# Optimization experiments

Measured on AMD Instinct MI355X. Metric: run time of the kernel, lower is better.

## Reference

```python
import jax, jax.numpy as jnp
import numpy as np

NUM_LEVELS = 4
RADIUS = 4


def _avg_pool2(x):
    # 2x2 stride-2 average pool over the last two dims of a 5D array, VALID padding
    s = jax.lax.reduce_window(x, 0.0, jax.lax.add, (1, 1, 1, 2, 2), (1, 1, 1, 2, 2), 'VALID')
    return s / 4.0


def _forward(fmap1, fmap2, coords):
    B, C, Hf, Wf = fmap1.shape
    _, N, _, H, W = coords.shape
    K = 2 * RADIUS + 1

    # all-pairs correlation: (B, H1, W1, H2, W2), scaled by 1/sqrt(C)
    f1 = fmap1.reshape(B, C, Hf * Wf)
    f2 = fmap2.reshape(B, C, Hf * Wf)
    corr = jnp.einsum('bcp,bcq->bpq', f1, f2) / jnp.sqrt(jnp.asarray(C, fmap1.dtype))
    corr = corr.reshape(B, Hf, Wf, Hf, Wf)

    pyramid = [corr]
    c = corr
    for _ in range(NUM_LEVELS - 1):
        c = _avg_pool2(c)
        pyramid.append(c)

    # coords channels: 0 = x, 1 = y  ->  (B, N, H, W, 2)
    cf = jnp.moveaxis(coords, 2, -1)

    d = jnp.linspace(-RADIUS, RADIUS, K, dtype=corr.dtype)
    # matches torch.stack(torch.meshgrid(dy, dx, indexing='ij'), axis=-1)
    delta = jnp.stack(jnp.meshgrid(d, d, indexing='ij'), axis=-1)  # (K, K, 2)

    bi = jnp.arange(B)[:, None, None, None, None]
    hi = jnp.arange(H)[None, None, :, None, None]
    wi = jnp.arange(W)[None, None, None, :, None]

    outs = []
    for i, cl in enumerate(pyramid):
        h2, w2 = cl.shape[-2], cl.shape[-1]
        # sampling coords (B, N, H, W, K, K, 2)
        sc = cf[..., None, None, :] / (2.0 ** i) + delta
        # grid_sample(align_corners=True) with coords pre-clamped to [-1,1]
        # == bilinear sample with pixel coords clamped to the valid range
        x = jnp.clip(sc[..., 0], 0.0, w2 - 1)
        y = jnp.clip(sc[..., 1], 0.0, h2 - 1)
        x0 = jnp.floor(x)
        y0 = jnp.floor(y)
        fx = (x - x0).reshape(B, N, H, W, K * K)
        fy = (y - y0).reshape(B, N, H, W, K * K)
        x0i = x0.astype(jnp.int32).reshape(B, N, H, W, K * K)
        y0i = y0.astype(jnp.int32).reshape(B, N, H, W, K * K)
        x1i = jnp.minimum(x0i + 1, w2 - 1)  # weight fx is 0 at the boundary
        y1i = jnp.minimum(y0i + 1, h2 - 1)

        cl_flat = cl.reshape(B, H, W, h2 * w2)  # query grid == feature grid (H==Hf, W==Wf)

        def gather(yi, xi):
            idx = yi * w2 + xi  # (B, N, H, W, K*K)
            return cl_flat[bi, hi, wi, idx]

        v = (gather(y0i, x0i) * (1 - fy) * (1 - fx)
             + gather(y0i, x1i) * (1 - fy) * fx
             + gather(y1i, x0i) * fy * (1 - fx)
             + gather(y1i, x1i) * fy * fx)
        outs.append(v)  # (B, N, H, W, K*K)

    out = jnp.concatenate(outs, axis=-1)  # (B, N, H, W, num_levels*K*K)
    # torch: (B,N,H,W,Cc).reshape(B, N*Cc, H, W) -- a raw row-major reshape
    out = out.reshape(B, N * out.shape[-1], H, W)
    return out.astype(jnp.float32)


def setup_inputs() -> dict:
    key = jax.random.key(0)
    k1, k2, k3 = jax.random.split(key, 3)
    B, C, H, W, N = 2, 256, 64, 64, 8
    fmap1 = jax.random.normal(k1, (B, C, H, W), dtype=jnp.float32)
    fmap2 = jax.random.normal(k2, (B, C, H, W), dtype=jnp.float32)
    coords = jax.random.uniform(k3, (B, N, 2, H, W), dtype=jnp.float32) * (W - 1)
    return {"fmap1": fmap1, "fmap2": fmap2, "coords": coords}


def reference(fmap1, fmap2, coords):
    return _forward(fmap1, fmap2, coords)
```

## Files before the change

kernel.cpp:

```cpp
#include <hip/hip_runtime.h>
#include <hip/hip_bf16.h>
#include <stdint.h>

#define B_   2
#define C_   256
#define P_   4096
#define N_   8
#define OUTC 2592

typedef __bf16 bf16x8 __attribute__((ext_vector_type(8)));
typedef float floatx4 __attribute__((ext_vector_type(4)));

__device__ __forceinline__ float bf2f(unsigned int u16) {
    union { unsigned int i; float f; } x; x.i = u16 << 16; return x.f;
}
__device__ __forceinline__ unsigned int f2bf(float f) {
    union { float f; unsigned int i; } x; x.f = f;
    unsigned int u = x.i + 0x7FFFu + ((x.i >> 16) & 1u);
    return u >> 16;
}

__global__ void conv_both(const float* __restrict__ in1, const float* __restrict__ in2,
                          __hip_bfloat16* __restrict__ out1, __hip_bfloat16* __restrict__ out2) {
    __shared__ float tile[32][33];
    int which = blockIdx.z >> 1;
    int b  = blockIdx.z & 1;
    const float* in = which ? in2 : in1;
    __hip_bfloat16* out = which ? out2 : out1;
    int p0 = blockIdx.x * 32;
    int c0 = blockIdx.y * 32;
    int tx = threadIdx.x;
    int ty0 = threadIdx.y;
    const float* ip = in + ((size_t)b * C_ + c0) * P_ + p0;
    for (int r = 0; r < 4; r++) {
        int ty = ty0 + r * 8;
        tile[ty][tx] = ip[(size_t)ty * P_ + tx];
    }
    __syncthreads();
    __hip_bfloat16* op = out + ((size_t)b * P_ + p0) * C_ + c0;
    for (int r = 0; r < 4; r++) {
        int ty = ty0 + r * 8;
        op[(size_t)ty * C_ + tx] = __float2bfloat16(tile[tx][ty]);
    }
}

__global__ __launch_bounds__(256) void gemm_corr(const __hip_bfloat16* __restrict__ A,
                                                 const __hip_bfloat16* __restrict__ Bm,
                                                 unsigned short* __restrict__ Cmat) {
    __shared__ __align__(16) __hip_bfloat16 lA[128 * 32];
    __shared__ __align__(16) __hip_bfloat16 lB[128 * 32];
    const int id = blockIdx.x;
    const int bz = id >> 10;
    const int r_ = id & 1023;
    const int s_ = r_ >> 3;
    const int by = (r_ & 7) * 4 + (s_ >> 5);
    const int bx = s_ & 31;
    const int m0 = by * 128;
    const int n0 = bx * 128;
    const __hip_bfloat16* Ab = A  + (size_t)bz * P_ * C_;
    const __hip_bfloat16* Bb = Bm + (size_t)bz * P_ * C_;
    unsigned short* Cb = Cmat + (size_t)bz * P_ * P_;

    const int tid  = threadIdx.x;
    const int lane = tid & 63;
    const int w    = tid >> 6;
    const int wm   = w & 1, wn = w >> 1;

    floatx4 acc[4][4];
    for (int i = 0; i < 4; i++)
        for (int j = 0; j < 4; j++)
            acc[i][j] = floatx4{0.f, 0.f, 0.f, 0.f};

    const int srow = w * 16 + (lane >> 2);
    const int scol = (lane & 3) * 8;

    for (int k0 = 0; k0 < C_; k0 += 32) {
        for (int j = 0; j < 2; j++) {
            int row = j * 64 + srow;
            const __hip_bfloat16* ga = Ab + (size_t)(m0 + row) * C_ + k0 + scol;
            const __hip_bfloat16* gb = Bb + (size_t)(n0 + row) * C_ + k0 + scol;
            __hip_bfloat16* la = lA + (j * 64 + w * 16) * 32;
            __hip_bfloat16* lb = lB + (j * 64 + w * 16) * 32;
            __builtin_amdgcn_global_load_lds((const __attribute__((address_space(1))) void*)ga,
                                             (__attribute__((address_space(3))) void*)la, 16, 0, 0);
            __builtin_amdgcn_global_load_lds((const __attribute__((address_space(1))) void*)gb,
                                             (__attribute__((address_space(3))) void*)lb, 16, 0, 0);
        }
        __syncthreads();
        const int kq   = (lane >> 4) * 8;
        const int rsel = lane & 15;
        bf16x8 af[4], bfv[4];
        for (int i = 0; i < 4; i++) {
            af[i]  = *(const bf16x8*)&lA[(wm * 64 + i * 16 + rsel) * 32 + kq];
            bfv[i] = *(const bf16x8*)&lB[(wn * 64 + i * 16 + rsel) * 32 + kq];
        }
        for (int i = 0; i < 4; i++)
            for (int j = 0; j < 4; j++)
                acc[i][j] = __builtin_amdgcn_mfma_f32_16x16x32_bf16(af[i], bfv[j], acc[i][j], 0, 0, 0);
        __syncthreads();
    }

    const float scale = 0.0625f;
    const int colb  = n0 + wn * 64 + (lane & 15);
    const int rbase = m0 + wm * 64 + ((lane >> 4) * 4);
    for (int i = 0; i < 4; i++)
        for (int j = 0; j < 4; j++)
            for (int r = 0; r < 4; r++)
                Cb[(size_t)(rbase + i * 16 + r) * P_ + colb + j * 16] =
                    (unsigned short)f2bf(acc[i][j][r] * scale);
}

__global__ __launch_bounds__(256) void pyramid(const unsigned int* __restrict__ c0,
                                               unsigned int* __restrict__ c1,
                                               unsigned int* __restrict__ c2,
                                               unsigned int* __restrict__ c3) {
    __shared__ unsigned int L0[2048];
    __shared__ unsigned int L1[512];
    __shared__ unsigned int L2[128];
    const int bp = blockIdx.x;
    const int tid = threadIdx.x;
    {
        const uint2* g = (const uint2*)(c0 + (size_t)bp * 2048);
        uint2* d = (uint2*)L0;
        for (int i = tid; i < 1024; i += 256) d[i] = g[i];
    }
    __syncthreads();
    for (int t = tid; t < 512; t += 256) {
        int x = t & 15;
        int y = t >> 4;
        unsigned int a = L0[(2 * y) * 32 + 2 * x];
        unsigned int a2 = L0[(2 * y) * 32 + 2 * x + 1];
        unsigned int b = L0[(2 * y + 1) * 32 + 2 * x];
        unsigned int b2 = L0[(2 * y + 1) * 32 + 2 * x + 1];
        float s0 = 0.25f * (bf2f(a & 0xffff) + bf2f(a >> 16) + bf2f(b & 0xffff) + bf2f(b >> 16));
        float s1 = 0.25f * (bf2f(a2 & 0xffff) + bf2f(a2 >> 16) + bf2f(b2 & 0xffff) + bf2f(b2 >> 16));
        unsigned int u = f2bf(s0) | (f2bf(s1) << 16);
        L1[t] = u;
        c1[(size_t)bp * 512 + t] = u;
    }
    __syncthreads();
    if (tid < 128) {
        int x = tid & 7;
        int y = tid >> 3;
        unsigned int a = L1[(2 * y) * 16 + 2 * x];
        unsigned int a2 = L1[(2 * y) * 16 + 2 * x + 1];
        unsigned int b = L1[(2 * y + 1) * 16 + 2 * x];
        unsigned int b2 = L1[(2 * y + 1) * 16 + 2 * x + 1];
        float s0 = 0.25f * (bf2f(a & 0xffff) + bf2f(a >> 16) + bf2f(b & 0xffff) + bf2f(b >> 16));
        float s1 = 0.25f * (bf2f(a2 & 0xffff) + bf2f(a2 >> 16) + bf2f(b2 & 0xffff) + bf2f(b2 >> 16));
        unsigned int u = f2bf(s0) | (f2bf(s1) << 16);
        L2[tid] = u;
        c2[(size_t)bp * 128 + tid] = u;
    }
    __syncthreads();
    if (tid < 32) {
        int x = tid & 3;
        int y = tid >> 2;
        unsigned int a = L2[(2 * y) * 8 + 2 * x];
        unsigned int a2 = L2[(2 * y) * 8 + 2 * x + 1];
        unsigned int b = L2[(2 * y + 1) * 8 + 2 * x];
        unsigned int b2 = L2[(2 * y + 1) * 8 + 2 * x + 1];
        float s0 = 0.25f * (bf2f(a & 0xffff) + bf2f(a >> 16) + bf2f(b & 0xffff) + bf2f(b >> 16));
        float s1 = 0.25f * (bf2f(a2 & 0xffff) + bf2f(a2 >> 16) + bf2f(b2 & 0xffff) + bf2f(b2 >> 16));
        c3[(size_t)bp * 32 + tid] = f2bf(s0) | (f2bf(s1) << 16);
    }
}

__global__ __launch_bounds__(256) void sample_k(const unsigned short* __restrict__ c0,
                                                const unsigned short* __restrict__ c1,
                                                const unsigned short* __restrict__ c2,
                                                const unsigned short* __restrict__ c3,
                                                const float* __restrict__ coords,
                                                float* __restrict__ outp) {
    __shared__ unsigned short sl16[5680];
    __shared__ float cs[16];
    __shared__ float2 xt[288];
    __shared__ float2 yt[288];
    __shared__ unsigned int ctb[324];

    const int bp = blockIdx.x;
    const int b  = bp >> 12;
    const int p  = bp & 4095;
    const int tid = threadIdx.x;
    unsigned int* slu = (unsigned int*)sl16;

    {
        const uint2* g0 = (const uint2*)(c0 + (size_t)bp * 4096);
        for (int i = tid; i < 1024; i += 256) {
            uint2 v = g0[i];
            int e = 4 * i;
            int y = e >> 6, x = e & 63;
            int u = (y * 66 + x) >> 1;
            slu[u] = v.x; slu[u + 1] = v.y;
        }
        const unsigned int* g1 = (const unsigned int*)(c1 + (size_t)bp * 1024);
        for (int i = tid; i < 512; i += 256)
            slu[2112 + (i >> 4) * 17 + (i & 15)] = g1[i];
        if (tid < 128)
            slu[2656 + (tid >> 3) * 9 + (tid & 7)] =
                ((const unsigned int*)(c2 + (size_t)bp * 256))[tid];
        if (tid < 32)
            slu[2800 + (tid >> 2) * 5 + (tid & 3)] =
                ((const unsigned int*)(c3 + (size_t)bp * 64))[tid];
        if (tid < 16) cs[tid] = coords[(size_t)(b * 16 + tid) * 4096 + p];
    }
    __syncthreads();

    for (int t = tid; t < 324; t += 256) {
        if (t < 288) {
            int n = t / 36, rem = t - n * 36;
            int l = rem / 9, dd = rem - l * 9;
            int wl = 64 >> l;
            int pw   = (l == 0) ? 66 : (l == 1) ? 34 : (l == 2) ? 18 : 10;
            int base = (l == 0) ? 0  : (l == 1) ? 4224 : (l == 2) ? 5312 : 5600;
            float inv = 1.0f / (float)(1 << l);
            float mx = (float)(wl - 1);
            float cx = cs[n * 2 + 0], cy = cs[n * 2 + 1];
            float xx = fminf(fmaxf(cx * inv + (float)(dd - 4), 0.0f), mx);
            float yy = fminf(fmaxf(cy * inv + (float)(dd - 4), 0.0f), mx);
            float x0f = floorf(xx), y0f = floorf(yy);
            int x0 = (int)x0f, y0 = (int)y0f;
            int x1 = min(x0 + 1, wl - 1), y1 = min(y0 + 1, wl - 1);
            unsigned int xb = (unsigned int)x0 | ((unsigned int)x1 << 8);
            unsigned int yb = (unsigned int)(base + y0 * pw)
                            | ((unsigned int)(base + y1 * pw) << 16);
            xt[t] = make_float2(xx - x0f, __uint_as_float(xb));
            yt[t] = make_float2(yy - y0f, __uint_as_float(yb));
        }
        int c = t;
        int l = c / 81, k = c - l * 81;
        int i9 = k / 9, j9 = k - i9 * 9;
        ctb[c] = ((unsigned int)(l * 9 + i9) << 8) | (unsigned int)(l * 9 + j9);
    }
    __syncthreads();

    const size_t outbase = (size_t)b * ((size_t)N_ * P_ * 324) + (size_t)p * 324;
    for (int o = tid; o < OUTC; o += 256) {
        int n = o / 324;
        int c = o - n * 324;
        unsigned int cv = ctb[c];
        int tb = n * 36;
        float2 xv = xt[tb + (cv >> 8)];
        float2 yv = yt[tb + (cv & 255)];
        unsigned int xb = __float_as_uint(xv.y);
        unsigned int yb = __float_as_uint(yv.y);
        int x0 = xb & 255, x1 = xb >> 8;
        int r0 = yb & 0xffff, r1 = yb >> 16;
        float fx = xv.x, fy = yv.x;
        float v00 = bf2f(sl16[r0 + x0]);
        float v01 = bf2f(sl16[r0 + x1]);
        float v10 = bf2f(sl16[r1 + x0]);
        float v11 = bf2f(sl16[r1 + x1]);
        float vx0 = v00 + fx * (v01 - v00);
        float vx1 = v10 + fx * (v11 - v10);
        float v   = vx0 + fy * (vx1 - vx0);
        outp[outbase + (size_t)n * (324 * 4095) + o] = v;
    }
}

extern "C" void kernel_launch(void* const* d_in, const int* in_sizes, int n_in,
                              void* d_out, int out_size, void* d_ws, size_t ws_size,
                              hipStream_t stream) {
    const float* fmap1  = (const float*)d_in[0];
    const float* fmap2  = (const float*)d_in[1];
    const float* coords = (const float*)d_in[2];
    float* out = (float*)d_out;

    char* ws = (char*)d_ws;
    size_t off = 0;
    auto alloc = [&](size_t bytes) {
        void* ptr = ws + off;
        off += (bytes + 255) & ~(size_t)255;
        return ptr;
    };
    __hip_bfloat16* f1t = (__hip_bfloat16*)alloc((size_t)B_ * P_ * C_ * 2);
    __hip_bfloat16* f2t = (__hip_bfloat16*)alloc((size_t)B_ * P_ * C_ * 2);
    unsigned short* corr0 = (unsigned short*)alloc((size_t)B_ * P_ * 4096 * 2);
    unsigned short* corr1 = (unsigned short*)alloc((size_t)B_ * P_ * 1024 * 2);
    unsigned short* corr2 = (unsigned short*)alloc((size_t)B_ * P_ * 256 * 2);
    unsigned short* corr3 = (unsigned short*)alloc((size_t)B_ * P_ * 64 * 2);

    conv_both<<<dim3(128, 8, 2 * B_), dim3(32, 8), 0, stream>>>(fmap1, fmap2, f1t, f2t);

    gemm_corr<<<dim3(2048), dim3(256), 0, stream>>>(f1t, f2t, corr0);

    pyramid<<<dim3(B_ * P_), dim3(256), 0, stream>>>((const unsigned int*)corr0,
                                                     (unsigned int*)corr1,
                                                     (unsigned int*)corr2,
                                                     (unsigned int*)corr3);

    sample_k<<<dim3(B_ * P_), dim3(256), 0, stream>>>(corr0, corr1, corr2, corr3, coords, out);
}
```

Baseline: 180.2 us.

## Fuse first pyramid pooling level into GEMM epilogue with packed bf16 stores

The correlation GEMM's warp tiling changes so each wave covers 32 rows by 128 columns, making horizontally adjacent column pairs reachable with a lane shuffle. The epilogue writes level-0 as packed 32-bit bf16 pairs and computes the level-1 2x2 average directly, so the pyramid kernel no longer rereads the full level-0 correlation volume. The remaining pyramid kernel only builds levels 2 and 3 from level 1. The sampling loop also replaces a per-iteration divide by 324 with an incremental counter. The level-1 value is now averaged from fp32 accumulators rather than rounded bf16, which slightly changes rounding.

```diff
diff --git a/kernel.cpp b/kernel.cpp
--- a/kernel.cpp
+++ b/kernel.cpp
@@ -46,7 +46,8 @@
 
 __global__ __launch_bounds__(256) void gemm_corr(const __hip_bfloat16* __restrict__ A,
                                                  const __hip_bfloat16* __restrict__ Bm,
-                                                 unsigned short* __restrict__ Cmat) {
+                                                 unsigned int* __restrict__ C0,
+                                                 unsigned short* __restrict__ C1) {
     __shared__ __align__(16) __hip_bfloat16 lA[128 * 32];
     __shared__ __align__(16) __hip_bfloat16 lB[128 * 32];
     const int id = blockIdx.x;
@@ -59,16 +60,14 @@
     const int n0 = bx * 128;
     const __hip_bfloat16* Ab = A  + (size_t)bz * P_ * C_;
     const __hip_bfloat16* Bb = Bm + (size_t)bz * P_ * C_;
-    unsigned short* Cb = Cmat + (size_t)bz * P_ * P_;
 
     const int tid  = threadIdx.x;
     const int lane = tid & 63;
     const int w    = tid >> 6;
-    const int wm   = w & 1, wn = w >> 1;
-
-    floatx4 acc[4][4];
-    for (int i = 0; i < 4; i++)
-        for (int j = 0; j < 4; j++)
+
+    floatx4 acc[2][8];
+    for (int i = 0; i < 2; i++)
+        for (int j = 0; j < 8; j++)
             acc[i][j] = floatx4{0.f, 0.f, 0.f, 0.f};
 
     const int srow = w * 16 + (lane >> 2);
@@ -89,62 +88,64 @@
         __syncthreads();
         const int kq   = (lane >> 4) * 8;
         const int rsel = lane & 15;
-        bf16x8 af[4], bfv[4];
-        for (int i = 0; i < 4; i++) {
-            af[i]  = *(const bf16x8*)&lA[(wm * 64 + i * 16 + rsel) * 32 + kq];
-            bfv[i] = *(const bf16x8*)&lB[(wn * 64 + i * 16 + rsel) * 32 + kq];
-        }
-        for (int i = 0; i < 4; i++)
-            for (int j = 0; j < 4; j++)
-                acc[i][j] = __builtin_amdgcn_mfma_f32_16x16x32_bf16(af[i], bfv[j], acc[i][j], 0, 0, 0);
+        bf16x8 af[2];
+        for (int i = 0; i < 2; i++)
+            af[i] = *(const bf16x8*)&lA[(w * 32 + i * 16 + rsel) * 32 + kq];
+        for (int jh = 0; jh < 2; jh++) {
+            bf16x8 bfv[4];
+            for (int jj = 0; jj < 4; jj++)
+                bfv[jj] = *(const bf16x8*)&lB[((jh * 4 + jj) * 16 + rsel) * 32 + kq];
+            for (int i = 0; i < 2; i++)
+                for (int jj = 0; jj < 4; jj++)
+                    acc[i][jh * 4 + jj] =
+                        __builtin_amdgcn_mfma_f32_16x16x32_bf16(af[i], bfv[jj],
+                                                                acc[i][jh * 4 + jj], 0, 0, 0);
+        }
         __syncthreads();
     }
 
     const float scale = 0.0625f;
-    const int colb  = n0 + wn * 64 + (lane & 15);
-    const int rbase = m0 + wm * 64 + ((lane >> 4) * 4);
-    for (int i = 0; i < 4; i++)
-        for (int j = 0; j < 4; j++)
-            for (int r = 0; r < 4; r++)
-                Cb[(size_t)(rbase + i * 16 + r) * P_ + colb + j * 16] =
-                    (unsigned short)f2bf(acc[i][j][r] * scale);
-}
-
-__global__ __launch_bounds__(256) void pyramid(const unsigned int* __restrict__ c0,
-                                               unsigned int* __restrict__ c1,
-                                               unsigned int* __restrict__ c2,
-                                               unsigned int* __restrict__ c3) {
-    __shared__ unsigned int L0[2048];
+    const int s15  = lane & 15;
+    const int even = (lane & 1) == 0;
+    for (int i = 0; i < 2; i++) {
+        for (int r = 0; r < 4; r++) {
+            int rp = m0 + w * 32 + i * 16 + ((lane >> 4) & 3) * 4 + r;
+            size_t rb0 = ((size_t)bz * P_ + rp) * 2048;
+            size_t rb1 = ((size_t)bz * P_ + rp) * 1024 + bx * 32;
+            for (int j = 0; j < 4; j++) {
+                float v0 = acc[i][j][r] * scale;
+                float v1 = acc[i][j + 4][r] * scale;
+                float v0n = __shfl_xor(v0, 1);
+                float v1n = __shfl_xor(v1, 1);
+                unsigned int u = even ? (f2bf(v0) | (f2bf(v0n) << 16))
+                                      : (f2bf(v1n) | (f2bf(v1) << 16));
+                int colu = even ? ((n0 + j * 16 + s15) >> 1)
+                                : ((n0 + j * 16 + 64 + s15 - 1) >> 1);
+                C0[rb0 + colu] = u;
+                if (even) {
+                    float s4 = (v0 + v0n + v1 + v1n) * 0.25f;
+                    C1[rb1 + ((j * 16 + s15) >> 1)] = (unsigned short)f2bf(s4);
+                }
+            }
+        }
+    }
+}
+
+__global__ __launch_bounds__(256) void pyr23(const unsigned int* __restrict__ c1,
+                                             unsigned int* __restrict__ c2,
+                                             unsigned int* __restrict__ c3) {
     __shared__ unsigned int L1[512];
     __shared__ unsigned int L2[128];
     const int bp = blockIdx.x;
     const int tid = threadIdx.x;
-    {
-        const uint2* g = (const uint2*)(c0 + (size_t)bp * 2048);
-        uint2* d = (uint2*)L0;
-        for (int i = tid; i < 1024; i += 256) d[i] = g[i];
-    }
-    __syncthreads();
-    for (int t = tid; t < 512; t += 256) {
-        int x = t & 15;
-        int y = t >> 4;
-        unsigned int a = L0[(2 * y) * 32 + 2 * x];
-        unsigned int a2 = L0[(2 * y) * 32 + 2 * x + 1];
-        unsigned int b = L0[(2 * y + 1) * 32 + 2 * x];
-        unsigned int b2 = L0[(2 * y + 1) * 32 + 2 * x + 1];
-        float s0 = 0.25f * (bf2f(a & 0xffff) + bf2f(a >> 16) + bf2f(b & 0xffff) + bf2f(b >> 16));
-        float s1 = 0.25f * (bf2f(a2 & 0xffff) + bf2f(a2 >> 16) + bf2f(b2 & 0xffff) + bf2f(b2 >> 16));
-        unsigned int u = f2bf(s0) | (f2bf(s1) << 16);
-        L1[t] = u;
-        c1[(size_t)bp * 512 + t] = u;
-    }
+    L1[tid]       = c1[(size_t)bp * 512 + tid];
+    L1[tid + 256] = c1[(size_t)bp * 512 + tid + 256];
     __syncthreads();
     if (tid < 128) {
-        int x = tid & 7;
-        int y = tid >> 3;
-        unsigned int a = L1[(2 * y) * 16 + 2 * x];
+        int x = tid & 7, y = tid >> 3;
+        unsigned int a  = L1[(2 * y) * 16 + 2 * x];
         unsigned int a2 = L1[(2 * y) * 16 + 2 * x + 1];
-        unsigned int b = L1[(2 * y + 1) * 16 + 2 * x];
+        unsigned int b  = L1[(2 * y + 1) * 16 + 2 * x];
         unsigned int b2 = L1[(2 * y + 1) * 16 + 2 * x + 1];
         float s0 = 0.25f * (bf2f(a & 0xffff) + bf2f(a >> 16) + bf2f(b & 0xffff) + bf2f(b >> 16));
         float s1 = 0.25f * (bf2f(a2 & 0xffff) + bf2f(a2 >> 16) + bf2f(b2 & 0xffff) + bf2f(b2 >> 16));
@@ -154,11 +155,10 @@
     }
     __syncthreads();
     if (tid < 32) {
-        int x = tid & 3;
-        int y = tid >> 2;
-        unsigned int a = L2[(2 * y) * 8 + 2 * x];
+        int x = tid & 3, y = tid >> 2;
+        unsigned int a  = L2[(2 * y) * 8 + 2 * x];
         unsigned int a2 = L2[(2 * y) * 8 + 2 * x + 1];
-        unsigned int b = L2[(2 * y + 1) * 8 + 2 * x];
+        unsigned int b  = L2[(2 * y + 1) * 8 + 2 * x];
         unsigned int b2 = L2[(2 * y + 1) * 8 + 2 * x + 1];
         float s0 = 0.25f * (bf2f(a & 0xffff) + bf2f(a >> 16) + bf2f(b & 0xffff) + bf2f(b >> 16));
         float s1 = 0.25f * (bf2f(a2 & 0xffff) + bf2f(a2 >> 16) + bf2f(b2 & 0xffff) + bf2f(b2 >> 16));
@@ -235,9 +235,8 @@
     __syncthreads();
 
     const size_t outbase = (size_t)b * ((size_t)N_ * P_ * 324) + (size_t)p * 324;
+    int n = 0, c = tid;
     for (int o = tid; o < OUTC; o += 256) {
-        int n = o / 324;
-        int c = o - n * 324;
         unsigned int cv = ctb[c];
         int tb = n * 36;
         float2 xv = xt[tb + (cv >> 8)];
@@ -255,6 +254,8 @@
         float vx1 = v10 + fx * (v11 - v10);
         float v   = vx0 + fy * (vx1 - vx0);
         outp[outbase + (size_t)n * (324 * 4095) + o] = v;
+        c += 256;
+        if (c >= 324) { c -= 324; n++; }
     }
 }
 
@@ -282,12 +283,12 @@
 
     conv_both<<<dim3(128, 8, 2 * B_), dim3(32, 8), 0, stream>>>(fmap1, fmap2, f1t, f2t);
 
-    gemm_corr<<<dim3(2048), dim3(256), 0, stream>>>(f1t, f2t, corr0);
-
-    pyramid<<<dim3(B_ * P_), dim3(256), 0, stream>>>((const unsigned int*)corr0,
-                                                     (unsigned int*)corr1,
-                                                     (unsigned int*)corr2,
-                                                     (unsigned int*)corr3);
+    gemm_corr<<<dim3(2048), dim3(256), 0, stream>>>(f1t, f2t,
+                                                    (unsigned int*)corr0, corr1);
+
+    pyr23<<<dim3(B_ * P_), dim3(256), 0, stream>>>((const unsigned int*)corr1,
+                                                   (unsigned int*)corr2,
+                                                   (unsigned int*)corr3);
 
     sample_k<<<dim3(B_ * P_), dim3(256), 0, stream>>>(corr0, corr1, corr2, corr3, coords, out);
 }
```

Result: faster. 175.9 us (-2.4%).

## Fuse correlation pyramid pooling into the sampling kernel via shared memory

Applied to the files above, without the earlier changes.

Removes the separate pyramid kernel and builds pooled levels 1-3 inside sample_k from the level-0 correlation tile already held in shared memory. This drops one launch plus the global write and reread of the pooled levels, and the second read of corr0. In exchange it adds two more block barriers and some pooling arithmetic per block. It also replaces the per-output division and modulo by 324 with an incremental counter.

```diff
diff --git a/kernel.cpp b/kernel.cpp
--- a/kernel.cpp
+++ b/kernel.cpp
@@ -110,66 +110,7 @@
                     (unsigned short)f2bf(acc[i][j][r] * scale);
 }
 
-__global__ __launch_bounds__(256) void pyramid(const unsigned int* __restrict__ c0,
-                                               unsigned int* __restrict__ c1,
-                                               unsigned int* __restrict__ c2,
-                                               unsigned int* __restrict__ c3) {
-    __shared__ unsigned int L0[2048];
-    __shared__ unsigned int L1[512];
-    __shared__ unsigned int L2[128];
-    const int bp = blockIdx.x;
-    const int tid = threadIdx.x;
-    {
-        const uint2* g = (const uint2*)(c0 + (size_t)bp * 2048);
-        uint2* d = (uint2*)L0;
-        for (int i = tid; i < 1024; i += 256) d[i] = g[i];
-    }
-    __syncthreads();
-    for (int t = tid; t < 512; t += 256) {
-        int x = t & 15;
-        int y = t >> 4;
-        unsigned int a = L0[(2 * y) * 32 + 2 * x];
-        unsigned int a2 = L0[(2 * y) * 32 + 2 * x + 1];
-        unsigned int b = L0[(2 * y + 1) * 32 + 2 * x];
-        unsigned int b2 = L0[(2 * y + 1) * 32 + 2 * x + 1];
-        float s0 = 0.25f * (bf2f(a & 0xffff) + bf2f(a >> 16) + bf2f(b & 0xffff) + bf2f(b >> 16));
-        float s1 = 0.25f * (bf2f(a2 & 0xffff) + bf2f(a2 >> 16) + bf2f(b2 & 0xffff) + bf2f(b2 >> 16));
-        unsigned int u = f2bf(s0) | (f2bf(s1) << 16);
-        L1[t] = u;
-        c1[(size_t)bp * 512 + t] = u;
-    }
-    __syncthreads();
-    if (tid < 128) {
-        int x = tid & 7;
-        int y = tid >> 3;
-        unsigned int a = L1[(2 * y) * 16 + 2 * x];
-        unsigned int a2 = L1[(2 * y) * 16 + 2 * x + 1];
-        unsigned int b = L1[(2 * y + 1) * 16 + 2 * x];
-        unsigned int b2 = L1[(2 * y + 1) * 16 + 2 * x + 1];
-        float s0 = 0.25f * (bf2f(a & 0xffff) + bf2f(a >> 16) + bf2f(b & 0xffff) + bf2f(b >> 16));
-        float s1 = 0.25f * (bf2f(a2 & 0xffff) + bf2f(a2 >> 16) + bf2f(b2 & 0xffff) + bf2f(b2 >> 16));
-        unsigned int u = f2bf(s0) | (f2bf(s1) << 16);
-        L2[tid] = u;
-        c2[(size_t)bp * 128 + tid] = u;
-    }
-    __syncthreads();
-    if (tid < 32) {
-        int x = tid & 3;
-        int y = tid >> 2;
-        unsigned int a = L2[(2 * y) * 8 + 2 * x];
-        unsigned int a2 = L2[(2 * y) * 8 + 2 * x + 1];
-        unsigned int b = L2[(2 * y + 1) * 8 + 2 * x];
-        unsigned int b2 = L2[(2 * y + 1) * 8 + 2 * x + 1];
-        float s0 = 0.25f * (bf2f(a & 0xffff) + bf2f(a >> 16) + bf2f(b & 0xffff) + bf2f(b >> 16));
-        float s1 = 0.25f * (bf2f(a2 & 0xffff) + bf2f(a2 >> 16) + bf2f(b2 & 0xffff) + bf2f(b2 >> 16));
-        c3[(size_t)bp * 32 + tid] = f2bf(s0) | (f2bf(s1) << 16);
-    }
-}
-
 __global__ __launch_bounds__(256) void sample_k(const unsigned short* __restrict__ c0,
-                                                const unsigned short* __restrict__ c1,
-                                                const unsigned short* __restrict__ c2,
-                                                const unsigned short* __restrict__ c3,
                                                 const float* __restrict__ coords,
                                                 float* __restrict__ outp) {
     __shared__ unsigned short sl16[5680];
@@ -193,19 +134,18 @@
             int u = (y * 66 + x) >> 1;
             slu[u] = v.x; slu[u + 1] = v.y;
         }
-        const unsigned int* g1 = (const unsigned int*)(c1 + (size_t)bp * 1024);
-        for (int i = tid; i < 512; i += 256)
-            slu[2112 + (i >> 4) * 17 + (i & 15)] = g1[i];
-        if (tid < 128)
-            slu[2656 + (tid >> 3) * 9 + (tid & 7)] =
-                ((const unsigned int*)(c2 + (size_t)bp * 256))[tid];
-        if (tid < 32)
-            slu[2800 + (tid >> 2) * 5 + (tid & 3)] =
-                ((const unsigned int*)(c3 + (size_t)bp * 64))[tid];
         if (tid < 16) cs[tid] = coords[(size_t)(b * 16 + tid) * 4096 + p];
     }
     __syncthreads();
 
+    for (int t = tid; t < 1024; t += 256) {
+        int y = t >> 5, x = t & 31;
+        unsigned int a = slu[y * 66 + x];
+        unsigned int c = slu[y * 66 + 33 + x];
+        float s = 0.25f * (bf2f(a & 0xffff) + bf2f(a >> 16)
+                         + bf2f(c & 0xffff) + bf2f(c >> 16));
+        sl16[4224 + y * 34 + x] = (unsigned short)f2bf(s);
+    }
     for (int t = tid; t < 324; t += 256) {
         if (t < 288) {
             int n = t / 36, rem = t - n * 36;
@@ -234,10 +174,29 @@
     }
     __syncthreads();
 
+    if (tid < 256) {
+        int y = tid >> 4, x = tid & 15;
+        unsigned int a = slu[2112 + 34 * y + x];
+        unsigned int c = slu[2112 + 34 * y + 17 + x];
+        float s = 0.25f * (bf2f(a & 0xffff) + bf2f(a >> 16)
+                         + bf2f(c & 0xffff) + bf2f(c >> 16));
+        sl16[5312 + y * 18 + x] = (unsigned short)f2bf(s);
+    }
+    __syncthreads();
+
+    if (tid < 64) {
+        int y = tid >> 3, x = tid & 7;
+        unsigned int a = slu[2656 + 18 * y + x];
+        unsigned int c = slu[2656 + 18 * y + 9 + x];
+        float s = 0.25f * (bf2f(a & 0xffff) + bf2f(a >> 16)
+                         + bf2f(c & 0xffff) + bf2f(c >> 16));
+        sl16[5600 + y * 10 + x] = (unsigned short)f2bf(s);
+    }
+    __syncthreads();
+
     const size_t outbase = (size_t)b * ((size_t)N_ * P_ * 324) + (size_t)p * 324;
+    int n = 0, c = tid;
     for (int o = tid; o < OUTC; o += 256) {
-        int n = o / 324;
-        int c = o - n * 324;
         unsigned int cv = ctb[c];
         int tb = n * 36;
         float2 xv = xt[tb + (cv >> 8)];
@@ -255,6 +214,8 @@
         float vx1 = v10 + fx * (v11 - v10);
         float v   = vx0 + fy * (vx1 - vx0);
         outp[outbase + (size_t)n * (324 * 4095) + o] = v;
+        c += 256;
+        if (c >= 324) { c -= 324; n++; }
     }
 }
 
@@ -276,18 +237,10 @@
     __hip_bfloat16* f1t = (__hip_bfloat16*)alloc((size_t)B_ * P_ * C_ * 2);
     __hip_bfloat16* f2t = (__hip_bfloat16*)alloc((size_t)B_ * P_ * C_ * 2);
     unsigned short* corr0 = (unsigned short*)alloc((size_t)B_ * P_ * 4096 * 2);
-    unsigned short* corr1 = (unsigned short*)alloc((size_t)B_ * P_ * 1024 * 2);
-    unsigned short* corr2 = (unsigned short*)alloc((size_t)B_ * P_ * 256 * 2);
-    unsigned short* corr3 = (unsigned short*)alloc((size_t)B_ * P_ * 64 * 2);
 
     conv_both<<<dim3(128, 8, 2 * B_), dim3(32, 8), 0, stream>>>(fmap1, fmap2, f1t, f2t);
 
     gemm_corr<<<dim3(2048), dim3(256), 0, stream>>>(f1t, f2t, corr0);
 
-    pyramid<<<dim3(B_ * P_), dim3(256), 0, stream>>>((const unsigned int*)corr0,
-                                                     (unsigned int*)corr1,
-                                                     (unsigned int*)corr2,
-                                                     (unsigned int*)corr3);
-
-    sample_k<<<dim3(B_ * P_), dim3(256), 0, stream>>>(corr0, corr1, corr2, corr3, coords, out);
-}
+    sample_k<<<dim3(B_ * P_), dim3(256), 0, stream>>>(corr0, coords, out);
+}
```

New measurement: 160.1 us. -11.1%, faster.
